# Kernel tuning notes

Measured on AMD Instinct MI355X. Metric: run time of the kernel, lower is better.

The kernel has to match this reference:

```python
import jax, jax.numpy as jnp
import numpy as np

B, S, W = 64, 128, 20
VOCAB, E, H = 256, 64, 256


def setup_inputs() -> dict:
    key = jax.random.key(0)
    ks = jax.random.split(key, 10)
    return {
        "chars": jax.random.randint(ks[0], (B, S, W), 0, VOCAB),
        "emb": jax.random.uniform(ks[1], (VOCAB, E), jnp.float32, -0.32, 0.32),
        "w1": jax.random.normal(ks[2], (H, E, 1), jnp.float32) * 0.1,
        "b1": jax.random.normal(ks[3], (H,), jnp.float32) * 0.1,
        "w3": jax.random.normal(ks[4], (H, E, 3), jnp.float32) * 0.1,
        "b3": jax.random.normal(ks[5], (H,), jnp.float32) * 0.1,
        "w5": jax.random.normal(ks[6], (H, E, 5), jnp.float32) * 0.1,
        "b5": jax.random.normal(ks[7], (H,), jnp.float32) * 0.1,
        "lw": jax.random.normal(ks[8], (H, 3 * H), jnp.float32) * 0.05,
        "lb": jax.random.normal(ks[9], (H,), jnp.float32) * 0.05,
    }


def _conv_relu_maxpool(x, w, b):
    # x: [N, E, W], w: [H, E, k] ('same' padding k//2) -> [N, H]
    k = w.shape[-1]
    pad = k // 2
    y = jax.lax.conv_general_dilated(
        x, w, window_strides=(1,), padding=[(pad, pad)],
        dimension_numbers=("NCH", "OIH", "NCH"))
    y = jax.nn.relu(y + b[None, :, None])
    return jnp.max(y, axis=2)  # global max over char positions


def reference(chars, emb, w1, b1, w3, b3, w5, b5, lw, lb):
    b, s, wlen = chars.shape
    flat = chars.reshape(-1, wlen)                 # [N, W]
    x = emb[flat]                                  # [N, W, E]
    x = jnp.transpose(x, (0, 2, 1))                # [N, E, W]
    outs = jnp.concatenate([
        _conv_relu_maxpool(x, w1, b1),
        _conv_relu_maxpool(x, w3, b3),
        _conv_relu_maxpool(x, w5, b5),
    ], axis=1)                                     # [N, 3H]
    out = outs @ lw.T + lb                         # [N, H]
    return out.reshape(b, s, -1)
```

## Files before the change

### kernel.cpp

```cpp
#include <hip/hip_runtime.h>
#include <hip/hip_bf16.h>

#define WW 20
#define NW 8192
#define VOCAB 256
#define EE 64
#define HH 256
#define K3 768
#define UNIT 2304

typedef short bf16x8 __attribute__((ext_vector_type(8)));
typedef float f32x4  __attribute__((ext_vector_type(4)));

__device__ __forceinline__ ushort f2bs(float x) {
    __hip_bfloat16 h = __float2bfloat16(x);
    union { __hip_bfloat16 h; ushort u; } c; c.h = h; return c.u;
}
__device__ __forceinline__ float blo(unsigned u) {
    union { unsigned i; float f; } c; c.i = u << 16; return c.f;
}
__device__ __forceinline__ float bhi(unsigned u) {
    union { unsigned i; float f; } c; c.i = u & 0xffff0000u; return c.f;
}
__device__ __forceinline__ unsigned pack2(float lo, float hi) {
    return (unsigned)f2bs(lo) | ((unsigned)f2bs(hi) << 16);
}

#define STEP(j, qq, t8v, a3, a5, mm1, mm3, mm5) {                        \
    float t0 = blo((qq).x), t1 = bhi((qq).x);                            \
    float t2 = blo((qq).y), t3 = bhi((qq).y);                            \
    float t4 = blo((qq).z), t5 = bhi((qq).z);                            \
    float t6 = blo((qq).w), t7 = bhi((qq).w);                            \
    mm1 = fmaxf(mm1, t0);                                                \
    if ((j) + 1 < WW) a3[((j)+1)%3] = t1;                                \
    a3[(j)%3] += t2;                                                     \
    if ((j) >= 1) { a3[((j)-1)%3] += t3;                                 \
                    mm3 = fmaxf(mm3, a3[((j)-1)%3]); }                   \
    if ((j) + 2 < WW) a5[((j)+2)%5] = t4;                                \
    if ((j) + 1 < WW) a5[((j)+1)%5] += t5;                               \
    a5[(j)%5] += t6;                                                     \
    if ((j) >= 1) a5[((j)-1)%5] += t7;                                   \
    if ((j) >= 2) { a5[((j)-2)%5] += (t8v);                              \
                    mm5 = fmaxf(mm5, a5[((j)-2)%5]); }                   \
}


__global__ __launch_bounds__(256) void prep(
        const float* __restrict__ w1,
        const float* __restrict__ w3,
        const float* __restrict__ w5,
        const float* __restrict__ lw,
        float* __restrict__ wTp,
        ushort* __restrict__ lwb) {
    const int bid = blockIdx.x;
    if (bid < 576) {
        int idx = bid * 256 + threadIdx.x;
        int e = idx / UNIT;
        int j = idx - e * UNIT;
        int s = j / 72, r = j - s * 72;
        int tap, h;
        if (r < 64) { tap = r & 7; h = s*8 + (r >> 3); }
        else        { tap = 8;     h = s*8 + (r - 64); }
        float v;
        if (tap == 0)      v = w1[h*EE + e];
        else if (tap <= 3) v = w3[(h*EE + e)*3 + (tap-1)];
        else               v = w5[(h*EE + e)*5 + (tap-4)];
        wTp[idx] = v;
    } else {
        int i = ((bid - 576) * 256 + threadIdx.x) * 4;
        float4 v = *(const float4*)(lw + i);
        ushort4 o4;
        o4.x = f2bs(v.x); o4.y = f2bs(v.y); o4.z = f2bs(v.z); o4.w = f2bs(v.w);
        *(ushort4*)(lwb + i) = o4;
    }
}

__global__ __launch_bounds__(256) void build_tables(
        const float* __restrict__ emb,
        const float* __restrict__ wTp,
        ushort* __restrict__ P5) {
    __shared__ float emb_s[4][EE];
    const int v0 = blockIdx.x * 4;
    const int j  = blockIdx.y * 256 + threadIdx.x;
    const int t  = threadIdx.x;
    emb_s[t >> 6][t & 63] = emb[v0*EE + t];
    __syncthreads();

    float a0 = 0.f, a1 = 0.f, a2 = 0.f, a3 = 0.f;
    const float* wp = wTp + j;
    #pragma unroll 8
    for (int e = 0; e < EE; ++e) {
        float w = wp[e * UNIT];
        a0 += emb_s[0][e] * w; a1 += emb_s[1][e] * w;
        a2 += emb_s[2][e] * w; a3 += emb_s[3][e] * w;
    }
    P5[(size_t)(v0+0)*UNIT + j] = f2bs(a0);
    P5[(size_t)(v0+1)*UNIT + j] = f2bs(a1);
    P5[(size_t)(v0+2)*UNIT + j] = f2bs(a2);
    P5[(size_t)(v0+3)*UNIT + j] = f2bs(a3);
}

__global__ __launch_bounds__(256) void conv_pool(
        const int* __restrict__ chars,
        const ushort* __restrict__ P5,
        const float* __restrict__ b1,
        const float* __restrict__ b3,
        const float* __restrict__ b5,
        ushort* __restrict__ outs) {
    __shared__ uint4 tileq[2304];
    const int t = threadIdx.x;
    const int g = blockIdx.x;
    const int s = blockIdx.y;

    {
        const char* src = (const char*)P5 + (size_t)s * 144;
        char* dst = (char*)tileq;
        #pragma unroll
        for (int i = 0; i < 9; ++i) {
            int c = i*256 + t;
            int v = c / 9, k = c - 9*v;
            *(uint4*)(dst + v*144 + k*16) =
                *(const uint4*)(src + (size_t)v*4608 + k*16);
        }
    }
    __syncthreads();

    const int p   = t & 3;
    const int wl0 = t >> 2;
    const char* tile = (const char*)tileq;
    const int h0  = s*8 + p*2;
    const float2 bb1 = *(const float2*)(b1 + h0);
    const float2 bb3 = *(const float2*)(b3 + h0);
    const float2 bb5 = *(const float2*)(b5 + h0);

    #pragma unroll
    for (int cc = 0; cc < 4; ++cc) {
        const int wl = cc*64 + wl0;
        const int n  = g*256 + wl;

        int cw[WW];
        {
            const int4* cp = (const int4*)(chars + n * WW);
            #pragma unroll
            for (int i = 0; i < 5; ++i) {
                int4 v = cp[i];
                cw[i*4+0] = v.x; cw[i*4+1] = v.y;
                cw[i*4+2] = v.z; cw[i*4+3] = v.w;
            }
        }

        float a3[2][3], a5[2][5], m1[2], m3[2], m5[2];
        #pragma unroll
        for (int i = 0; i < 2; ++i) {
            a3[i][0] = 0.f; a5[i][0] = 0.f; a5[i][1] = 0.f;
            m1[i] = -1e30f; m3[i] = -1e30f; m5[i] = -1e30f;
        }

        uint4 qa[2], qb[2]; unsigned t8[2];
        {
            int c0 = cw[0];
            qa[0] = *(const uint4*)(tile + c0*144 + p*32);
            qb[0] = *(const uint4*)(tile + c0*144 + p*32 + 16);
            t8[0] = *(const unsigned*)(tile + c0*144 + 128 + p*4);
        }

        #pragma unroll
        for (int j = 0; j < WW; ++j) {
            const int cur = j & 1, nxt = cur ^ 1;
            if (j + 1 < WW) {
                int cn = cw[j+1];
                qa[nxt] = *(const uint4*)(tile + cn*144 + p*32);
                qb[nxt] = *(const uint4*)(tile + cn*144 + p*32 + 16);
                t8[nxt] = *(const unsigned*)(tile + cn*144 + 128 + p*4);
            }
            float t8lo = blo(t8[cur]), t8hi = bhi(t8[cur]);
            STEP(j, qa[cur], t8lo, a3[0], a5[0], m1[0], m3[0], m5[0]);
            STEP(j, qb[cur], t8hi, a3[1], a5[1], m1[1], m3[1], m5[1]);
        }
        #pragma unroll
        for (int i = 0; i < 2; ++i) {
            m3[i] = fmaxf(m3[i], a3[i][(WW-1)%3]);
            m5[i] = fmaxf(m5[i], a5[i][(WW-2)%5]);
            m5[i] = fmaxf(m5[i], a5[i][(WW-1)%5]);
        }

        unsigned* op = (unsigned*)(outs + (size_t)n * K3 + h0);
        op[0*(HH/2)] = pack2(fmaxf(m1[0]+bb1.x, 0.f), fmaxf(m1[1]+bb1.y, 0.f));
        op[1*(HH/2)] = pack2(fmaxf(m3[0]+bb3.x, 0.f), fmaxf(m3[1]+bb3.y, 0.f));
        op[2*(HH/2)] = pack2(fmaxf(m5[0]+bb5.x, 0.f), fmaxf(m5[1]+bb5.y, 0.f));
    }
}

__global__ __launch_bounds__(64) void gemm_out(
        const ushort* __restrict__ outs,
        const ushort* __restrict__ lwb,
        const float* __restrict__ lb,
        float* __restrict__ out) {
    const int lane = threadIdx.x;
    const int m0 = blockIdx.x * 32;
    const int n0 = blockIdx.y * 32;
    const int mrow = lane & 15, quad = lane >> 4;

    f32x4 acc00 = (f32x4){0,0,0,0}, acc01 = (f32x4){0,0,0,0};
    f32x4 acc10 = (f32x4){0,0,0,0}, acc11 = (f32x4){0,0,0,0};
    const ushort* ap = outs + (size_t)(m0 + mrow) * K3 + quad * 8;
    const ushort* bp = lwb  + (size_t)(n0 + mrow) * K3 + quad * 8;

    bf16x8 A0[4], A1[4], B0[4], B1[4];
    #pragma unroll
    for (int pi = 0; pi < 3; ++pi) {
        A0[pi] = *(const bf16x8*)(ap + pi*32);
        A1[pi] = *(const bf16x8*)(ap + 16*K3 + pi*32);
        B0[pi] = *(const bf16x8*)(bp + pi*32);
        B1[pi] = *(const bf16x8*)(bp + 16*K3 + pi*32);
    }

    #pragma unroll
    for (int it = 0; it < K3/32; ++it) {
        const int sl = it & 3;
        const int nl = (it + 3) & 3;
        const int kn = (it + 3 < K3/32) ? (it + 3) * 32 : 0;
        A0[nl] = *(const bf16x8*)(ap + kn);
        A1[nl] = *(const bf16x8*)(ap + 16*K3 + kn);
        B0[nl] = *(const bf16x8*)(bp + kn);
        B1[nl] = *(const bf16x8*)(bp + 16*K3 + kn);
        acc00 = __builtin_amdgcn_mfma_f32_16x16x32_bf16(A0[sl], B0[sl], acc00, 0, 0, 0);
        acc01 = __builtin_amdgcn_mfma_f32_16x16x32_bf16(A0[sl], B1[sl], acc01, 0, 0, 0);
        acc10 = __builtin_amdgcn_mfma_f32_16x16x32_bf16(A1[sl], B0[sl], acc10, 0, 0, 0);
        acc11 = __builtin_amdgcn_mfma_f32_16x16x32_bf16(A1[sl], B1[sl], acc11, 0, 0, 0);
    }

    #pragma unroll
    for (int i = 0; i < 2; ++i) {
        #pragma unroll
        for (int jn = 0; jn < 2; ++jn) {
            const f32x4 acc = (i==0) ? (jn==0 ? acc00 : acc01)
                                     : (jn==0 ? acc10 : acc11);
            int ncol = n0 + jn*16 + mrow;
            float lbv = lb[ncol];
            #pragma unroll
            for (int r = 0; r < 4; ++r)
                out[(size_t)(m0 + i*16 + quad*4 + r)*HH + ncol] = acc[r] + lbv;
        }
    }
}

extern "C" void kernel_launch(void* const* d_in, const int* in_sizes, int n_in,
                              void* d_out, int out_size, void* d_ws, size_t ws_size,
                              hipStream_t stream) {
    const int*   chars = (const int*)d_in[0];
    const float* emb   = (const float*)d_in[1];
    const float* w1    = (const float*)d_in[2];
    const float* b1    = (const float*)d_in[3];
    const float* w3    = (const float*)d_in[4];
    const float* b3    = (const float*)d_in[5];
    const float* w5    = (const float*)d_in[6];
    const float* b5    = (const float*)d_in[7];
    const float* lw    = (const float*)d_in[8];
    const float* lb    = (const float*)d_in[9];

    ushort* P5   = (ushort*)d_ws;
    float*  wTp  = (float*)(P5 + VOCAB * UNIT);
    ushort* outs = (ushort*)(wTp + EE * UNIT);
    ushort* lwb  = outs + (size_t)NW * K3;

    prep<<<768, 256, 0, stream>>>(w1, w3, w5, lw, wTp, lwb);
    build_tables<<<dim3(VOCAB/4, 9), 256, 0, stream>>>(emb, wTp, P5);
    conv_pool<<<dim3(NW/256, 32), 256, 0, stream>>>(chars, P5, b1, b3, b5, outs);
    gemm_out<<<dim3(NW/32, HH/32), 64, 0, stream>>>(outs, lwb, lb, (float*)d_out);
}
```

Baseline: 131.7 us.

## Remap conv_pool threads to one channel each and prescale char indices

conv_pool now gives each of 8 lanes one output channel (16B + 2B LDS reads per char) instead of 4 lanes handling two channels each, and loops over 8 word chunks instead of 4. The char indices are pre-multiplied by the 144-byte tile stride in an extra prep section, so the inner loop skips the multiply. A launch-bounds occupancy hint of 4 is added. The remap halves per-thread registers and accumulator work but doubles reloads of the chars rows and switches output stores to 2-byte scattered writes.

```diff
diff --git a/kernel.cpp b/kernel.cpp
--- a/kernel.cpp
+++ b/kernel.cpp
@@ -21,9 +21,6 @@
 }
 __device__ __forceinline__ float bhi(unsigned u) {
     union { unsigned i; float f; } c; c.i = u & 0xffff0000u; return c.f;
-}
-__device__ __forceinline__ unsigned pack2(float lo, float hi) {
-    return (unsigned)f2bs(lo) | ((unsigned)f2bs(hi) << 16);
 }
 
 #define STEP(j, qq, t8v, a3, a5, mm1, mm3, mm5) {                        \
@@ -46,12 +43,14 @@
 
 
 __global__ __launch_bounds__(256) void prep(
+        const int* __restrict__ chars,
         const float* __restrict__ w1,
         const float* __restrict__ w3,
         const float* __restrict__ w5,
         const float* __restrict__ lw,
         float* __restrict__ wTp,
-        ushort* __restrict__ lwb) {
+        ushort* __restrict__ lwb,
+        int* __restrict__ csb) {
     const int bid = blockIdx.x;
     if (bid < 576) {
         int idx = bid * 256 + threadIdx.x;
@@ -66,12 +65,15 @@
         else if (tap <= 3) v = w3[(h*EE + e)*3 + (tap-1)];
         else               v = w5[(h*EE + e)*5 + (tap-4)];
         wTp[idx] = v;
-    } else {
+    } else if (bid < 768) {
         int i = ((bid - 576) * 256 + threadIdx.x) * 4;
         float4 v = *(const float4*)(lw + i);
         ushort4 o4;
         o4.x = f2bs(v.x); o4.y = f2bs(v.y); o4.z = f2bs(v.z); o4.w = f2bs(v.w);
         *(ushort4*)(lwb + i) = o4;
+    } else {
+        int i = (bid - 768) * 256 + threadIdx.x;
+        csb[i] = chars[i] * 144;
     }
 }
 
@@ -100,8 +102,8 @@
     P5[(size_t)(v0+3)*UNIT + j] = f2bs(a3);
 }
 
-__global__ __launch_bounds__(256) void conv_pool(
-        const int* __restrict__ chars,
+__global__ __launch_bounds__(256, 4) void conv_pool(
+        const int* __restrict__ csb,
         const ushort* __restrict__ P5,
         const float* __restrict__ b1,
         const float* __restrict__ b3,
@@ -125,22 +127,21 @@
     }
     __syncthreads();
 
-    const int p   = t & 3;
-    const int wl0 = t >> 2;
-    const char* tile = (const char*)tileq;
-    const int h0  = s*8 + p*2;
-    const float2 bb1 = *(const float2*)(b1 + h0);
-    const float2 bb3 = *(const float2*)(b3 + h0);
-    const float2 bb5 = *(const float2*)(b5 + h0);
-
-    #pragma unroll
-    for (int cc = 0; cc < 4; ++cc) {
-        const int wl = cc*64 + wl0;
+    const int r   = t & 7;
+    const int wl0 = t >> 3;
+    const char* tileQ = (const char*)tileq + r*16;
+    const char* tileT = (const char*)tileq + 128 + r*2;
+    const int h = s*8 + r;
+    const float bb1 = b1[h], bb3 = b3[h], bb5 = b5[h];
+
+    #pragma unroll
+    for (int cc = 0; cc < 8; ++cc) {
+        const int wl = cc*32 + wl0;
         const int n  = g*256 + wl;
 
         int cw[WW];
         {
-            const int4* cp = (const int4*)(chars + n * WW);
+            const int4* cp = (const int4*)(csb + n * WW);
             #pragma unroll
             for (int i = 0; i < 5; ++i) {
                 int4 v = cp[i];
@@ -149,45 +150,32 @@
             }
         }
 
-        float a3[2][3], a5[2][5], m1[2], m3[2], m5[2];
-        #pragma unroll
-        for (int i = 0; i < 2; ++i) {
-            a3[i][0] = 0.f; a5[i][0] = 0.f; a5[i][1] = 0.f;
-            m1[i] = -1e30f; m3[i] = -1e30f; m5[i] = -1e30f;
-        }
-
-        uint4 qa[2], qb[2]; unsigned t8[2];
-        {
-            int c0 = cw[0];
-            qa[0] = *(const uint4*)(tile + c0*144 + p*32);
-            qb[0] = *(const uint4*)(tile + c0*144 + p*32 + 16);
-            t8[0] = *(const unsigned*)(tile + c0*144 + 128 + p*4);
-        }
+        float a3[3], a5[5], m1, m3, m5;
+        a3[0] = 0.f; a5[0] = 0.f; a5[1] = 0.f;
+        m1 = -1e30f; m3 = -1e30f; m5 = -1e30f;
+
+        uint4 q[2]; ushort t8[2];
+        q[0]  = *(const uint4*)(tileQ + cw[0]);
+        t8[0] = *(const ushort*)(tileT + cw[0]);
 
         #pragma unroll
         for (int j = 0; j < WW; ++j) {
             const int cur = j & 1, nxt = cur ^ 1;
             if (j + 1 < WW) {
-                int cn = cw[j+1];
-                qa[nxt] = *(const uint4*)(tile + cn*144 + p*32);
-                qb[nxt] = *(const uint4*)(tile + cn*144 + p*32 + 16);
-                t8[nxt] = *(const unsigned*)(tile + cn*144 + 128 + p*4);
+                q[nxt]  = *(const uint4*)(tileQ + cw[j+1]);
+                t8[nxt] = *(const ushort*)(tileT + cw[j+1]);
             }
-            float t8lo = blo(t8[cur]), t8hi = bhi(t8[cur]);
-            STEP(j, qa[cur], t8lo, a3[0], a5[0], m1[0], m3[0], m5[0]);
-            STEP(j, qb[cur], t8hi, a3[1], a5[1], m1[1], m3[1], m5[1]);
-        }
-        #pragma unroll
-        for (int i = 0; i < 2; ++i) {
-            m3[i] = fmaxf(m3[i], a3[i][(WW-1)%3]);
-            m5[i] = fmaxf(m5[i], a5[i][(WW-2)%5]);
-            m5[i] = fmaxf(m5[i], a5[i][(WW-1)%5]);
-        }
-
-        unsigned* op = (unsigned*)(outs + (size_t)n * K3 + h0);
-        op[0*(HH/2)] = pack2(fmaxf(m1[0]+bb1.x, 0.f), fmaxf(m1[1]+bb1.y, 0.f));
-        op[1*(HH/2)] = pack2(fmaxf(m3[0]+bb3.x, 0.f), fmaxf(m3[1]+bb3.y, 0.f));
-        op[2*(HH/2)] = pack2(fmaxf(m5[0]+bb5.x, 0.f), fmaxf(m5[1]+bb5.y, 0.f));
+            float t8v = blo(t8[cur]);
+            STEP(j, q[cur], t8v, a3, a5, m1, m3, m5);
+        }
+        m3 = fmaxf(m3, a3[(WW-1)%3]);
+        m5 = fmaxf(m5, a5[(WW-2)%5]);
+        m5 = fmaxf(m5, a5[(WW-1)%5]);
+
+        ushort* op = outs + (size_t)n * K3 + h;
+        op[0*HH] = f2bs(fmaxf(m1 + bb1, 0.f));
+        op[1*HH] = f2bs(fmaxf(m3 + bb3, 0.f));
+        op[2*HH] = f2bs(fmaxf(m5 + bb5, 0.f));
     }
 }
 
@@ -263,9 +251,10 @@
     float*  wTp  = (float*)(P5 + VOCAB * UNIT);
     ushort* outs = (ushort*)(wTp + EE * UNIT);
     ushort* lwb  = outs + (size_t)NW * K3;
-
-    prep<<<768, 256, 0, stream>>>(w1, w3, w5, lw, wTp, lwb);
+    int*    csb  = (int*)(lwb + (size_t)VOCAB * K3);
+
+    prep<<<1408, 256, 0, stream>>>(chars, w1, w3, w5, lw, wTp, lwb, csb);
     build_tables<<<dim3(VOCAB/4, 9), 256, 0, stream>>>(emb, wTp, P5);
-    conv_pool<<<dim3(NW/256, 32), 256, 0, stream>>>(chars, P5, b1, b3, b5, outs);
+    conv_pool<<<dim3(NW/256, 32), 256, 0, stream>>>(csb, P5, b1, b3, b5, outs);
     gemm_out<<<dim3(NW/32, HH/32), 64, 0, stream>>>(outs, lwb, lb, (float*)d_out);
 }
```

After: 130.1 us (median of 2 runs). About the same (-1.3%).
